# Optimization experiments

Measured on AMD Instinct MI355X. Metric: run time of the kernel, lower is better.

## Reference

```python
import jax, jax.numpy as jnp
import numpy as np

NUM_GROUP = 512   # init kwarg num_group
GROUP_SIZE = 32   # init kwarg group_size
B, N, C = 8, 8192, 6


def setup_inputs() -> dict:
    key = jax.random.key(0)
    xyz = jax.random.normal(key, (B, N, C), dtype=jnp.float32)
    return {"xyz": xyz}


def _fps_indices(pts, num_group):
    b, n, _ = pts.shape
    first = jnp.zeros((b,), dtype=jnp.int32)
    dist = jnp.sum((pts - pts[:, :1]) ** 2, axis=-1)  # [B, N] dist to point 0

    def step(dist, _):
        far = jnp.argmax(dist, axis=1).astype(jnp.int32)            # [B]
        newp = jnp.take_along_axis(pts, far[:, None, None], axis=1)  # [B,1,3]
        d = jnp.sum((pts - newp) ** 2, axis=-1)
        return jnp.minimum(dist, d), far

    _, rest = jax.lax.scan(step, dist, None, length=num_group - 1)  # [G-1, B]
    return jnp.concatenate([first[None, :], rest], axis=0).T        # [B, G]


def reference(xyz):
    batch_size, num_points, c = xyz.shape
    xyz_only = xyz[:, :, :3]
    extra = xyz[:, :, 3:] if c > 3 else None

    # FPS centers
    fps_idx = _fps_indices(xyz_only, NUM_GROUP)                       # [B, G]
    center = jnp.take_along_axis(xyz_only, fps_idx[:, :, None], axis=1)  # [B, G, 3]

    # KNN: squared distances center->all points, [B, G, N]
    d2 = (jnp.sum(center ** 2, -1)[:, :, None]
          + jnp.sum(xyz_only ** 2, -1)[:, None, :]
          - 2.0 * jnp.einsum('bgc,bnc->bgn', center, xyz_only))
    _, idx = jax.lax.top_k(-d2, GROUP_SIZE)                           # [B, G, K] ascending dist
    idx = idx.astype(jnp.int32)

    # Gather neighborhoods (batched gather == flattened idx_base trick in torch)
    idx_g = idx.reshape(batch_size, NUM_GROUP * GROUP_SIZE)
    neigh_xyz = jnp.take_along_axis(xyz_only, idx_g[:, :, None], axis=1)
    neigh_xyz = neigh_xyz.reshape(batch_size, NUM_GROUP, GROUP_SIZE, 3)
    rel = neigh_xyz - center[:, :, None, :]
    if extra is not None:
        neigh_extra = jnp.take_along_axis(extra, idx_g[:, :, None], axis=1)
        neigh_extra = neigh_extra.reshape(batch_size, NUM_GROUP, GROUP_SIZE, -1)
        neighborhood = jnp.concatenate([rel, neigh_extra], axis=-1)
    else:
        neighborhood = rel
    return neighborhood, center, idx
```

## Files before the change

kernel.cpp:

```cpp
#include <hip/hip_runtime.h>
#include <hip/hip_bf16.h>

#define NB 8
#define NP 8192
#define NC 6
#define NG 512
#define GS 32

#define CENTER_OFF (NB * NG * GS * NC)
#define IDX_OFF    (CENTER_OFF + NB * NG * 3)


#define DPP_MAX_U32(v, ctrl)                                               \
  {                                                                        \
    unsigned _m = (unsigned)__builtin_amdgcn_update_dpp(                   \
        (int)(v), (int)(v), (ctrl), 0xf, 0xf, false);                      \
    (v) = (_m > (v)) ? _m : (v);                                           \
  }
#define DPP_MIN_U32(v, ctrl)                                               \
  {                                                                        \
    unsigned _m = (unsigned)__builtin_amdgcn_update_dpp(                   \
        (int)(v), (int)(v), (ctrl), 0xf, 0xf, false);                      \
    (v) = (_m < (v)) ? _m : (v);                                           \
  }

__global__ __launch_bounds__(512) void fps_kernel(
    const float* __restrict__ xyz, float* __restrict__ out,
    int* __restrict__ cidx)
{
  __shared__ float4 mir[NP];
  __shared__ unsigned long long kpart[2][8];
  __shared__ int sel[NG];

  const int b = blockIdx.x;
  const int tid = threadIdx.x;
  const int lane = tid & 63;
  const int wave = tid >> 6;
  const float* base = xyz + (size_t)b * NP * NC;

  float px[16], py[16], pz[16], dv[16];
  unsigned int LO[16];
#pragma unroll
  for (int j = 0; j < 16; ++j) {
    const int p = tid + (j << 9);
    px[j] = base[p * 6 + 0];
    py[j] = base[p * 6 + 1];
    pz[j] = base[p * 6 + 2];
    mir[p] = make_float4(px[j], py[j], pz[j], 0.0f);
    LO[j] = (unsigned)(NP - 1 - p);
  }
  if (tid == 0) sel[0] = 0;
  __syncthreads();

  float4 c0 = mir[0];
  float cx = c0.x, cy = c0.y, cz = c0.z;

#pragma unroll
  for (int j = 0; j < 16; ++j) {
    const float dx = __fsub_rn(px[j], cx);
    const float dy = __fsub_rn(py[j], cy);
    const float dz = __fsub_rn(pz[j], cz);
    dv[j] = __fadd_rn(
        __fadd_rn(__fmul_rn(dx, dx), __fmul_rn(dy, dy)), __fmul_rn(dz, dz));
  }

  for (int it = 1; it < NG; ++it) {
    unsigned long long t[16];
#pragma unroll
    for (int j = 0; j < 16; ++j)
      t[j] = ((unsigned long long)__float_as_uint(dv[j]) << 32) | LO[j];
#pragma unroll
    for (int s = 8; s; s >>= 1)
#pragma unroll
      for (int j = 0; j < s; ++j)
        t[j] = t[j] > t[j + s] ? t[j] : t[j + s];
    const unsigned sv = (unsigned)(t[0] >> 32);
    const unsigned lo = (unsigned)t[0];

    unsigned r = sv;
    DPP_MAX_U32(r, 0x111); DPP_MAX_U32(r, 0x112); DPP_MAX_U32(r, 0x114);
    DPP_MAX_U32(r, 0x118); DPP_MAX_U32(r, 0x142); DPP_MAX_U32(r, 0x143);
    const unsigned smax = (unsigned)__builtin_amdgcn_readlane((int)r, 63);

    const unsigned long long m = __ballot(sv == smax);
    unsigned wlo;
    if (m & (m - 1)) {
      unsigned long long mm = m; unsigned best = 0;
      while (mm) {
        const int l = __builtin_ctzll(mm);
        const unsigned c = (unsigned)__builtin_amdgcn_readlane((int)lo, l);
        if (c > best) best = c;
        mm &= mm - 1;
      }
      wlo = best;
    } else {
      wlo = (unsigned)__builtin_amdgcn_readlane((int)lo, __builtin_ctzll(m));
    }

    const int pb = it & 1;
    if (lane == 0)
      kpart[pb][wave] = ((unsigned long long)smax << 32) | wlo;
    __syncthreads();

    const unsigned long long* kp = kpart[pb];
    unsigned long long g0 = kp[0] > kp[1] ? kp[0] : kp[1];
    unsigned long long g1 = kp[2] > kp[3] ? kp[2] : kp[3];
    unsigned long long g2 = kp[4] > kp[5] ? kp[4] : kp[5];
    unsigned long long g3 = kp[6] > kp[7] ? kp[6] : kp[7];
    g0 = g0 > g1 ? g0 : g1;
    g2 = g2 > g3 ? g2 : g3;
    g0 = g0 > g2 ? g0 : g2;
    const int gi = (NP - 1) - (int)(unsigned)(g0 & 0xFFFFFFFFu);
    if (tid == 0) sel[it] = gi;

    const float4 c = mir[gi];
    cx = c.x; cy = c.y; cz = c.z;

#pragma unroll
    for (int j = 0; j < 16; ++j) {
      const float dx = __fsub_rn(px[j], cx);
      const float dy = __fsub_rn(py[j], cy);
      const float dz = __fsub_rn(pz[j], cz);
      const float d = __fadd_rn(
          __fadd_rn(__fmul_rn(dx, dx), __fmul_rn(dy, dy)), __fmul_rn(dz, dz));
      dv[j] = fminf(dv[j], d);
    }
  }
  __syncthreads();

  {
    const int p = sel[tid];
    const float4 c = mir[p];
    const size_t cb = (size_t)(b * NG + tid) * 3;
    out[CENTER_OFF + cb + 0] = c.x;
    out[CENTER_OFF + cb + 1] = c.y;
    out[CENTER_OFF + cb + 2] = c.z;
    cidx[b * NG + tid] = p;
  }
}

__global__ __launch_bounds__(256) void knn_kernel(
    const float* __restrict__ xyz, float* __restrict__ out,
    const int* __restrict__ cidx)
{
  __shared__ unsigned bins[2048];
  __shared__ unsigned part[256];
  __shared__ int sB;
  __shared__ unsigned wcnt, ccnt;
  __shared__ unsigned long long wbuf[32];
  __shared__ unsigned long long cbuf[224];
  __shared__ int widx[GS];

  const int bg = blockIdx.x;
  const int b = bg >> 9;
  const int tid = threadIdx.x;
  const int lane = tid & 63;
  const int wave = tid >> 6;
  const float* base = xyz + (size_t)b * NP * NC;

  const int pc = cidx[bg] & (NP - 1);
  const float cx = base[pc * 6 + 0];
  const float cy = base[pc * 6 + 1];
  const float cz = base[pc * 6 + 2];
  const float cc = __fadd_rn(
      __fadd_rn(__fmul_rn(cx, cx), __fmul_rn(cy, cy)), __fmul_rn(cz, cz));

  for (int i = tid; i < 2048; i += 256) bins[i] = 0;
  if (tid == 0) { wcnt = 0; ccnt = 0; }
  __syncthreads();

  unsigned fv[32];
#pragma unroll
  for (int j = 0; j < 32; ++j) {
    const int p = tid + (j << 8);
    const float x = base[p * 6 + 0];
    const float y = base[p * 6 + 1];
    const float z = base[p * 6 + 2];
    const float xx = __fadd_rn(
        __fadd_rn(__fmul_rn(x, x), __fmul_rn(y, y)), __fmul_rn(z, z));
    const float dot = __fadd_rn(
        __fadd_rn(__fmul_rn(cx, x), __fmul_rn(cy, y)), __fmul_rn(cz, z));
    const float d2 = __fsub_rn(__fadd_rn(cc, xx), __fmul_rn(2.0f, dot));
    unsigned u = __float_as_uint(d2);
    u ^= ((unsigned)((int)u >> 31)) | 0x80000000u;
    fv[j] = u;
    atomicAdd(&bins[u >> 21], 1u);
  }
  __syncthreads();

  unsigned s = 0;
#pragma unroll
  for (int i = 0; i < 8; ++i) s += bins[tid * 8 + i];
  part[tid] = s;
  __syncthreads();

  if (wave == 0) {
    const unsigned q = part[4 * lane + 0] + part[4 * lane + 1] +
                       part[4 * lane + 2] + part[4 * lane + 3];
    unsigned cum = q;
#pragma unroll
    for (int off = 1; off < 64; off <<= 1) {
      const unsigned t = __shfl_up(cum, (unsigned)off);
      if (lane >= off) cum += t;
    }
    const unsigned long long mb = __ballot(cum >= 32u);
    const int ls = __builtin_ctzll(mb);
    unsigned run = (unsigned)__builtin_amdgcn_readlane((int)cum, ls) -
                   (unsigned)__builtin_amdgcn_readlane((int)q, ls);
    const int t0 = 4 * ls;
    const unsigned p0 = part[t0 + 0], p1 = part[t0 + 1];
    const unsigned p2 = part[t0 + 2], p3 = part[t0 + 3];
    int ti = t0;
    if (run + p0 < 32u) {
      run += p0; ti = t0 + 1;
      if (run + p1 < 32u) {
        run += p1; ti = t0 + 2;
        if (run + p2 < 32u) { run += p2; ti = t0 + 3; (void)p3; }
      }
    }
    const int bb = ti * 8;
    unsigned h[8];
#pragma unroll
    for (int i = 0; i < 8; ++i) h[i] = bins[bb + i];
    int B = bb;
    for (int i = 0; i < 8; ++i) {
      if (run + h[i] >= 32u) { B = bb + i; break; }
      run += h[i];
    }
    if (lane == 0) sB = B;
  }
  __syncthreads();
  const int B = sB;

#pragma unroll
  for (int j = 0; j < 32; ++j) {
    const int bin = (int)(fv[j] >> 21);
    if (bin <= B) {
      const unsigned long long key =
          ((unsigned long long)fv[j] << 32) | (unsigned)(tid + (j << 8));
      if (bin < B) {
        const unsigned pos = atomicAdd(&wcnt, 1u);
        if (pos < 32u) wbuf[pos] = key;
      } else {
        const unsigned pos = atomicAdd(&ccnt, 1u);
        if (pos < 224u) cbuf[pos] = key;
      }
    }
  }
  __syncthreads();

  if (wave == 0) {
    const int W = (int)wcnt;
    const int C = (int)ccnt;
    unsigned long long pool[4];
#pragma unroll
    for (int rr = 0; rr < 4; ++rr) {
      const int i = lane + (rr << 6);
      unsigned long long k = ~0ull;
      if (i < W) k = wbuf[i];
      else if (i - W < C && i - W < 224) k = cbuf[i - W];
      pool[rr] = k;
    }
    unsigned long long l0 = pool[0] < pool[1] ? pool[0] : pool[1];
    unsigned long long l1 = pool[2] < pool[3] ? pool[2] : pool[3];
    unsigned long long loc = l0 < l1 ? l0 : l1;

    unsigned long long mykey = 0;
    for (int k = 0; k < GS; ++k) {
      const unsigned hi = (unsigned)(loc >> 32);
      unsigned r = hi;
      DPP_MIN_U32(r, 0x111); DPP_MIN_U32(r, 0x112); DPP_MIN_U32(r, 0x114);
      DPP_MIN_U32(r, 0x118); DPP_MIN_U32(r, 0x142); DPP_MIN_U32(r, 0x143);
      const unsigned minhi = (unsigned)__builtin_amdgcn_readlane((int)r, 63);

      const unsigned long long m = __ballot(hi == minhi);
      unsigned lo;
      if (m & (m - 1)) {
        unsigned long long mm = m; unsigned best = 0xFFFFFFFFu;
        while (mm) {
          const int l = __builtin_ctzll(mm);
          const unsigned c =
              (unsigned)__builtin_amdgcn_readlane((int)(unsigned)loc, l);
          if (c < best) best = c;
          mm &= mm - 1;
        }
        lo = best;
      } else {
        lo = (unsigned)__builtin_amdgcn_readlane((int)(unsigned)loc,
                                                 __builtin_ctzll(m));
      }
      const unsigned long long win = ((unsigned long long)minhi << 32) | lo;
      if (lane == k) mykey = win;
      if (loc == win) {
#pragma unroll
        for (int rr = 0; rr < 4; ++rr)
          if (pool[rr] == win) pool[rr] = ~0ull;
        l0 = pool[0] < pool[1] ? pool[0] : pool[1];
        l1 = pool[2] < pool[3] ? pool[2] : pool[3];
        loc = l0 < l1 ? l0 : l1;
      }
    }
    if (lane < GS) widx[lane] = (int)(unsigned)(mykey & 0xFFFFFFFFu);
  }
  __syncthreads();

  if (tid < GS) {
    const int p = widx[tid] & (NP - 1);
    const float v0 = base[p * 6 + 0];
    const float v1 = base[p * 6 + 1];
    const float v2 = base[p * 6 + 2];
    const size_t ob = ((size_t)bg * GS + tid) * 6;
    out[ob + 0] = __fsub_rn(v0, cx);
    out[ob + 1] = __fsub_rn(v1, cy);
    out[ob + 2] = __fsub_rn(v2, cz);
    out[ob + 3] = base[p * 6 + 3];
    out[ob + 4] = base[p * 6 + 4];
    out[ob + 5] = base[p * 6 + 5];
    out[IDX_OFF + (size_t)bg * GS + tid] = (float)p;
  }
}

extern "C" void kernel_launch(void* const* d_in, const int* in_sizes, int n_in,
                              void* d_out, int out_size, void* d_ws,
                              size_t ws_size, hipStream_t stream)
{
  const float* xyz = (const float*)d_in[0];
  float* out = (float*)d_out;
  int* cidx = (int*)d_ws;

  hipLaunchKernelGGL(fps_kernel, dim3(NB), dim3(512), 0, stream,
                     xyz, out, cidx);
  hipLaunchKernelGGL(knn_kernel, dim3(NB * NG), dim3(256), 0, stream,
                     xyz, out, cidx);
}
```

Before: 663.9 us.

## Halve FPS block size, use float argmax, add two-level radix select in KNN

The FPS kernel now runs 256 threads holding 32 points each. Its per-iteration argmax compares plain floats and then recovers the winning index with a scan, replacing the 64-bit packed key reductions, which leaves fewer waves to combine per iteration. The KNN kernel adds a second 11-bit histogram pass over the boundary bin so the candidate pool is narrower, and it clamps the buffer counts. The extra histogram pass, the additional barriers and higher register pressure in FPS are the costs.

```diff
diff --git a/kernel.cpp b/kernel.cpp
--- a/kernel.cpp
+++ b/kernel.cpp
@@ -24,12 +24,12 @@
     (v) = (_m < (v)) ? _m : (v);                                           \
   }
 
-__global__ __launch_bounds__(512) void fps_kernel(
+__global__ __launch_bounds__(256) void fps_kernel(
     const float* __restrict__ xyz, float* __restrict__ out,
     int* __restrict__ cidx)
 {
   __shared__ float4 mir[NP];
-  __shared__ unsigned long long kpart[2][8];
+  __shared__ unsigned long long kpart[2][4];
   __shared__ int sel[NG];
 
   const int b = blockIdx.x;
@@ -38,16 +38,14 @@
   const int wave = tid >> 6;
   const float* base = xyz + (size_t)b * NP * NC;
 
-  float px[16], py[16], pz[16], dv[16];
-  unsigned int LO[16];
-#pragma unroll
-  for (int j = 0; j < 16; ++j) {
-    const int p = tid + (j << 9);
+  float px[32], py[32], pz[32], dv[32];
+#pragma unroll
+  for (int j = 0; j < 32; ++j) {
+    const int p = tid + (j << 8);
     px[j] = base[p * 6 + 0];
     py[j] = base[p * 6 + 1];
     pz[j] = base[p * 6 + 2];
     mir[p] = make_float4(px[j], py[j], pz[j], 0.0f);
-    LO[j] = (unsigned)(NP - 1 - p);
   }
   if (tid == 0) sel[0] = 0;
   __syncthreads();
@@ -56,7 +54,7 @@
   float cx = c0.x, cy = c0.y, cz = c0.z;
 
 #pragma unroll
-  for (int j = 0; j < 16; ++j) {
+  for (int j = 0; j < 32; ++j) {
     const float dx = __fsub_rn(px[j], cx);
     const float dy = __fsub_rn(py[j], cy);
     const float dz = __fsub_rn(pz[j], cz);
@@ -65,27 +63,30 @@
   }
 
   for (int it = 1; it < NG; ++it) {
-    unsigned long long t[16];
-#pragma unroll
-    for (int j = 0; j < 16; ++j)
-      t[j] = ((unsigned long long)__float_as_uint(dv[j]) << 32) | LO[j];
+    float t[16];
+#pragma unroll
+    for (int j = 0; j < 16; ++j) t[j] = fmaxf(dv[j], dv[j + 16]);
 #pragma unroll
     for (int s = 8; s; s >>= 1)
 #pragma unroll
-      for (int j = 0; j < s; ++j)
-        t[j] = t[j] > t[j + s] ? t[j] : t[j + s];
-    const unsigned sv = (unsigned)(t[0] >> 32);
-    const unsigned lo = (unsigned)t[0];
-
+      for (int j = 0; j < s; ++j) t[j] = fmaxf(t[j], t[j + s]);
+    const float m = t[0];
+    int jj = 0;
+#pragma unroll
+    for (int j = 31; j >= 0; --j)
+      if (dv[j] == m) jj = j;
+    const unsigned lo = (unsigned)(NP - 1 - tid - (jj << 8));
+
+    const unsigned sv = __float_as_uint(m);
     unsigned r = sv;
     DPP_MAX_U32(r, 0x111); DPP_MAX_U32(r, 0x112); DPP_MAX_U32(r, 0x114);
     DPP_MAX_U32(r, 0x118); DPP_MAX_U32(r, 0x142); DPP_MAX_U32(r, 0x143);
     const unsigned smax = (unsigned)__builtin_amdgcn_readlane((int)r, 63);
 
-    const unsigned long long m = __ballot(sv == smax);
+    const unsigned long long mk = __ballot(sv == smax);
     unsigned wlo;
-    if (m & (m - 1)) {
-      unsigned long long mm = m; unsigned best = 0;
+    if (mk & (mk - 1)) {
+      unsigned long long mm = mk; unsigned best = 0;
       while (mm) {
         const int l = __builtin_ctzll(mm);
         const unsigned c = (unsigned)__builtin_amdgcn_readlane((int)lo, l);
@@ -94,7 +95,7 @@
       }
       wlo = best;
     } else {
-      wlo = (unsigned)__builtin_amdgcn_readlane((int)lo, __builtin_ctzll(m));
+      wlo = (unsigned)__builtin_amdgcn_readlane((int)lo, __builtin_ctzll(mk));
     }
 
     const int pb = it & 1;
@@ -105,11 +106,7 @@
     const unsigned long long* kp = kpart[pb];
     unsigned long long g0 = kp[0] > kp[1] ? kp[0] : kp[1];
     unsigned long long g1 = kp[2] > kp[3] ? kp[2] : kp[3];
-    unsigned long long g2 = kp[4] > kp[5] ? kp[4] : kp[5];
-    unsigned long long g3 = kp[6] > kp[7] ? kp[6] : kp[7];
     g0 = g0 > g1 ? g0 : g1;
-    g2 = g2 > g3 ? g2 : g3;
-    g0 = g0 > g2 ? g0 : g2;
     const int gi = (NP - 1) - (int)(unsigned)(g0 & 0xFFFFFFFFu);
     if (tid == 0) sel[it] = gi;
 
@@ -117,7 +114,7 @@
     cx = c.x; cy = c.y; cz = c.z;
 
 #pragma unroll
-    for (int j = 0; j < 16; ++j) {
+    for (int j = 0; j < 32; ++j) {
       const float dx = __fsub_rn(px[j], cx);
       const float dy = __fsub_rn(py[j], cy);
       const float dz = __fsub_rn(pz[j], cz);
@@ -128,14 +125,14 @@
   }
   __syncthreads();
 
-  {
-    const int p = sel[tid];
+  for (int g = tid; g < NG; g += 256) {
+    const int p = sel[g];
     const float4 c = mir[p];
-    const size_t cb = (size_t)(b * NG + tid) * 3;
+    const size_t cb = (size_t)(b * NG + g) * 3;
     out[CENTER_OFF + cb + 0] = c.x;
     out[CENTER_OFF + cb + 1] = c.y;
     out[CENTER_OFF + cb + 2] = c.z;
-    cidx[b * NG + tid] = p;
+    cidx[b * NG + g] = p;
   }
 }
 
@@ -145,7 +142,7 @@
 {
   __shared__ unsigned bins[2048];
   __shared__ unsigned part[256];
-  __shared__ int sB;
+  __shared__ int sB, sRun;
   __shared__ unsigned wcnt, ccnt;
   __shared__ unsigned long long wbuf[32];
   __shared__ unsigned long long cbuf[224];
@@ -188,12 +185,13 @@
   }
   __syncthreads();
 
-  unsigned s = 0;
-#pragma unroll
-  for (int i = 0; i < 8; ++i) s += bins[tid * 8 + i];
-  part[tid] = s;
-  __syncthreads();
-
+  {
+    unsigned s = 0;
+#pragma unroll
+    for (int i = 0; i < 8; ++i) s += bins[tid * 8 + i];
+    part[tid] = s;
+  }
+  __syncthreads();
   if (wave == 0) {
     const unsigned q = part[4 * lane + 0] + part[4 * lane + 1] +
                        part[4 * lane + 2] + part[4 * lane + 3];
@@ -207,40 +205,76 @@
     const int ls = __builtin_ctzll(mb);
     unsigned run = (unsigned)__builtin_amdgcn_readlane((int)cum, ls) -
                    (unsigned)__builtin_amdgcn_readlane((int)q, ls);
-    const int t0 = 4 * ls;
-    const unsigned p0 = part[t0 + 0], p1 = part[t0 + 1];
-    const unsigned p2 = part[t0 + 2], p3 = part[t0 + 3];
-    int ti = t0;
-    if (run + p0 < 32u) {
-      run += p0; ti = t0 + 1;
-      if (run + p1 < 32u) {
-        run += p1; ti = t0 + 2;
-        if (run + p2 < 32u) { run += p2; ti = t0 + 3; (void)p3; }
-      }
-    }
-    const int bb = ti * 8;
-    unsigned h[8];
-#pragma unroll
-    for (int i = 0; i < 8; ++i) h[i] = bins[bb + i];
-    int B = bb;
-    for (int i = 0; i < 8; ++i) {
-      if (run + h[i] >= 32u) { B = bb + i; break; }
+    unsigned h[32];
+#pragma unroll
+    for (int i = 0; i < 32; ++i) h[i] = bins[(ls << 5) + i];
+    int T = ls << 5;
+#pragma unroll
+    for (int i = 0; i < 32; ++i) {
+      if (run + h[i] >= 32u) { T = (ls << 5) + i; break; }
       run += h[i];
     }
-    if (lane == 0) sB = B;
-  }
-  __syncthreads();
-  const int B = sB;
+    if (lane == 0) { sB = T; sRun = (int)run; }
+  }
+  __syncthreads();
+  const int B1 = sB;
+  const unsigned run1 = (unsigned)sRun;
+  const unsigned r2 = 32u - run1;
+  __syncthreads();
+
+  for (int i = tid; i < 2048; i += 256) bins[i] = 0;
+  __syncthreads();
+#pragma unroll
+  for (int j = 0; j < 32; ++j)
+    if ((int)(fv[j] >> 21) == B1) atomicAdd(&bins[(fv[j] >> 10) & 0x7FF], 1u);
+  __syncthreads();
+  {
+    unsigned s = 0;
+#pragma unroll
+    for (int i = 0; i < 8; ++i) s += bins[tid * 8 + i];
+    part[tid] = s;
+  }
+  __syncthreads();
+  if (wave == 0) {
+    const unsigned q = part[4 * lane + 0] + part[4 * lane + 1] +
+                       part[4 * lane + 2] + part[4 * lane + 3];
+    unsigned cum = q;
+#pragma unroll
+    for (int off = 1; off < 64; off <<= 1) {
+      const unsigned t = __shfl_up(cum, (unsigned)off);
+      if (lane >= off) cum += t;
+    }
+    const unsigned long long mb = __ballot(cum >= r2);
+    const int ls = __builtin_ctzll(mb);
+    unsigned run = (unsigned)__builtin_amdgcn_readlane((int)cum, ls) -
+                   (unsigned)__builtin_amdgcn_readlane((int)q, ls);
+    unsigned h[32];
+#pragma unroll
+    for (int i = 0; i < 32; ++i) h[i] = bins[(ls << 5) + i];
+    int T = ls << 5;
+#pragma unroll
+    for (int i = 0; i < 32; ++i) {
+      if (run + h[i] >= r2) { T = (ls << 5) + i; break; }
+      run += h[i];
+    }
+    if (lane == 0) { sB = T; sRun = (int)run; }
+  }
+  __syncthreads();
+  const int B2 = sB;
+  const unsigned key22 = ((unsigned)B1 << 11) | (unsigned)B2;
 
 #pragma unroll
   for (int j = 0; j < 32; ++j) {
-    const int bin = (int)(fv[j] >> 21);
-    if (bin <= B) {
+    const unsigned hi11 = fv[j] >> 21;
+    const unsigned top22 = fv[j] >> 10;
+    if (top22 <= key22) {
       const unsigned long long key =
           ((unsigned long long)fv[j] << 32) | (unsigned)(tid + (j << 8));
-      if (bin < B) {
-        const unsigned pos = atomicAdd(&wcnt, 1u);
-        if (pos < 32u) wbuf[pos] = key;
+      if (top22 < key22) {
+        if ((int)hi11 < B1 || hi11 == (unsigned)B1) {
+          const unsigned pos = atomicAdd(&wcnt, 1u);
+          if (pos < 32u) wbuf[pos] = key;
+        }
       } else {
         const unsigned pos = atomicAdd(&ccnt, 1u);
         if (pos < 224u) cbuf[pos] = key;
@@ -250,15 +284,15 @@
   __syncthreads();
 
   if (wave == 0) {
-    const int W = (int)wcnt;
-    const int C = (int)ccnt;
+    const int W = (int)(wcnt < 32u ? wcnt : 32u);
+    const int C = (int)(ccnt < 224u ? ccnt : 224u);
     unsigned long long pool[4];
 #pragma unroll
     for (int rr = 0; rr < 4; ++rr) {
       const int i = lane + (rr << 6);
       unsigned long long k = ~0ull;
       if (i < W) k = wbuf[i];
-      else if (i - W < C && i - W < 224) k = cbuf[i - W];
+      else if (i - W < C) k = cbuf[i - W];
       pool[rr] = k;
     }
     unsigned long long l0 = pool[0] < pool[1] ? pool[0] : pool[1];
@@ -328,7 +362,7 @@
   float* out = (float*)d_out;
   int* cidx = (int*)d_ws;
 
-  hipLaunchKernelGGL(fps_kernel, dim3(NB), dim3(512), 0, stream,
+  hipLaunchKernelGGL(fps_kernel, dim3(NB), dim3(256), 0, stream,
                      xyz, out, cidx);
   hipLaunchKernelGGL(knn_kernel, dim3(NB * NG), dim3(256), 0, stream,
                      xyz, out, cidx);
```

Measured after the change: 620.3 us. -6.6%, faster.
